# Performance work log

Hardware: AMD Instinct MI355X
Metric: run time of the kernel (lower is better)

Reference implementation:

```python
import jax, jax.numpy as jnp
import numpy as np

MARGIN = 0.2
W_HARD = 1.0
W_SOFT = 0.0
NORMALIZE = True
PD_EPS = 1e-6  # torch F.pairwise_distance eps used inside TripletMarginLoss


def setup_inputs() -> dict:
    key = jax.random.key(0)
    k1, k2, k3 = jax.random.split(key, 3)
    N, D = 8192, 128
    z = jax.random.normal(k1, (N, D), dtype=jnp.float32)
    labels = jax.random.randint(k2, (N,), 0, 16, dtype=jnp.int32)
    subjects = jax.random.randint(k3, (N,), 0, 32, dtype=jnp.int32)
    return {"z": z, "labels": labels, "subjects": subjects}


def _batch_hard(z, pos_mask, neg_mask, margin):
    # pairwise euclidean distances (cdist p=2); mining indices are ints, so
    # stop_gradient keeps vjp clean (matches torch: argmax/argmin detach).
    sq = jnp.sum(z * z, axis=1)
    d2 = sq[:, None] + sq[None, :] - 2.0 * (z @ z.T)
    dist = jax.lax.stop_gradient(jnp.sqrt(jnp.maximum(d2, 0.0)))
    inf = jnp.asarray(jnp.inf, dist.dtype)
    p_idx = jnp.argmax(jnp.where(pos_mask, dist, -inf), axis=1)  # hardest positive
    n_idx = jnp.argmin(jnp.where(neg_mask, dist, inf), axis=1)   # hardest negative
    valid = jnp.any(pos_mask, axis=1) & jnp.any(neg_mask, axis=1)
    a, p, n = z, z[p_idx], z[n_idx]
    d_ap = jnp.sqrt(jnp.sum((a - p + PD_EPS) ** 2, axis=1))
    d_an = jnp.sqrt(jnp.sum((a - n + PD_EPS) ** 2, axis=1))
    per = jnp.maximum(d_ap - d_an + margin, 0.0)
    cnt = jnp.sum(valid)
    loss = jnp.sum(per * valid) / jnp.maximum(cnt, 1).astype(per.dtype)
    return jnp.where(cnt > 0, loss, 0.0)


def reference(z, labels, subjects):
    if NORMALIZE:
        z = z / jnp.maximum(jnp.linalg.norm(z, axis=1, keepdims=True), 1e-12)
    N = z.shape[0]
    same_class = labels[:, None] == labels[None, :]
    same_subj = subjects[:, None] == subjects[None, :]
    not_eye = ~jnp.eye(N, dtype=bool)
    loss = 0.0
    denom = 0.0
    if W_HARD != 0:
        pos_hard = same_class & ~same_subj & not_eye
        neg_hard = ~same_class & same_subj & not_eye
        loss = loss + W_HARD * _batch_hard(z, pos_hard, neg_hard, MARGIN)
        denom += abs(W_HARD)
    if W_SOFT != 0:
        pos_soft = same_class & same_subj & not_eye
        neg_soft = ~same_class & ~same_subj & not_eye
        loss = loss + W_SOFT * _batch_hard(z, pos_soft, neg_soft, MARGIN)
        denom += abs(W_SOFT)
    return loss / max(denom, 1e-12)
```

## Files before the change

### kernel.cpp

```cpp
#include <hip/hip_runtime.h>
#include <math.h>

#define N 8192
#define D 128
#define MARGIN 0.2f
#define PD_EPS 1e-6f
#define NCHUNK 16
#define CHUNKJ (N / NCHUNK)

typedef __attribute__((ext_vector_type(8))) short bf16x8;
typedef __attribute__((ext_vector_type(4))) float f32x4;

__device__ __forceinline__ unsigned short f2bf(float f) {
    unsigned u = __float_as_uint(f);
    u += 0x7FFFu + ((u >> 16) & 1u);
    return (unsigned short)(u >> 16);
}
__device__ __forceinline__ unsigned umn(unsigned a, unsigned b) { return a < b ? a : b; }
__device__ __forceinline__ unsigned umx(unsigned a, unsigned b) { return a > b ? a : b; }

__global__ __launch_bounds__(256) void k_normalize(const float* __restrict__ z,
                                                   const int* __restrict__ labels,
                                                   const int* __restrict__ subjects,
                                                   unsigned short* __restrict__ znb,
                                                   float* __restrict__ invn,
                                                   int* __restrict__ meta) {
    int row  = blockIdx.x * 4 + (threadIdx.x >> 6);
    int lane = threadIdx.x & 63;
    float2 v = ((const float2*)(z + (size_t)row * D))[lane];
    float ss = v.x * v.x + v.y * v.y;
    #pragma unroll
    for (int m = 1; m < 64; m <<= 1) ss += __shfl_xor(ss, m, 64);
    float norm = fmaxf(sqrtf(ss), 1e-12f);
    float ox = v.x / norm, oy = v.y / norm;
    ushort2 b; b.x = f2bf(ox); b.y = f2bf(oy);
    ((ushort2*)(znb + (size_t)row * D))[lane] = b;
    if (lane == 0) {
        invn[row] = 1.0f / norm;
        meta[row] = labels[row] * 32 + subjects[row];
    }
}

__global__ __launch_bounds__(256, 2) void k_mine(const unsigned short* __restrict__ znb,
                                                 const int* __restrict__ meta,
                                                 unsigned* __restrict__ posk,
                                                 unsigned* __restrict__ negk) {
    const int wave = threadIdx.x >> 6;
    const int lane = threadIdx.x & 63;
    const int m    = lane & 15;
    const int quad = lane >> 4;
    const int iw   = (blockIdx.x * 4 + wave) * 64;
    const int jc   = blockIdx.y;
    const int jbase = jc * CHUNKJ;

    bf16x8 afrag[4][4];
    #pragma unroll
    for (int u = 0; u < 4; ++u)
        #pragma unroll
        for (int s = 0; s < 4; ++s)
            afrag[u][s] = *(const bf16x8*)(znb + (size_t)(iw + u * 16 + m) * D + s * 32 + quad * 8);

    int mi[16];
    #pragma unroll
    for (int u = 0; u < 4; ++u)
        #pragma unroll
        for (int r = 0; r < 4; ++r)
            mi[u * 4 + r] = meta[iw + u * 16 + quad * 4 + r];

    unsigned bp[16], bn[16];
    #pragma unroll
    for (int s = 0; s < 16; ++s) { bp[s] = 0xFFFFFFFFu; bn[s] = 0u; }

    for (int t = 0; t < CHUNKJ / 64; ++t) {
        const int jt = jbase + t * 64;

        f32x4 acc[4][4];
        #pragma unroll
        for (int u = 0; u < 4; ++u)
            #pragma unroll
            for (int v = 0; v < 4; ++v)
                acc[u][v] = (f32x4){0.f, 0.f, 0.f, 0.f};

        #pragma unroll
        for (int s = 0; s < 4; ++s) {
            bf16x8 bf[4];
            #pragma unroll
            for (int v = 0; v < 4; ++v)
                bf[v] = *(const bf16x8*)(znb + (size_t)(jt + v * 16 + m) * D + s * 32 + quad * 8);
            #pragma unroll
            for (int u = 0; u < 4; ++u)
                #pragma unroll
                for (int v = 0; v < 4; ++v)
                    acc[u][v] = __builtin_amdgcn_mfma_f32_16x16x32_bf16(afrag[u][s], bf[v], acc[u][v], 0, 0, 0);
        }

        #pragma unroll
        for (int v = 0; v < 4; ++v) {
            const int jv  = jt + v * 16 + m;
            const int mjv = meta[jv];
            #pragma unroll
            for (int u = 0; u < 4; ++u)
                #pragma unroll
                for (int r = 0; r < 4; ++r) {
                    float dot = acc[u][v][r];
                    unsigned key = (__float_as_uint(dot + 2.0f) & 0xFFFFE000u) | (unsigned)jv;
                    int x = mi[u * 4 + r] ^ mjv;
                    bool pos = (x != 0) && (x < 32);
                    bool neg = (x != 0) && ((x & 31) == 0);
                    bp[u * 4 + r] = umn(bp[u * 4 + r], pos ? key : 0xFFFFFFFFu);
                    bn[u * 4 + r] = umx(bn[u * 4 + r], neg ? key : 0u);
                }
        }
    }

    #pragma unroll
    for (int mm = 1; mm < 16; mm <<= 1)
        #pragma unroll
        for (int s = 0; s < 16; ++s) {
            bp[s] = umn(bp[s], (unsigned)__shfl_xor((int)bp[s], mm, 64));
            bn[s] = umx(bn[s], (unsigned)__shfl_xor((int)bn[s], mm, 64));
        }
    if (m == 0) {
        #pragma unroll
        for (int u = 0; u < 4; ++u)
            #pragma unroll
            for (int r = 0; r < 4; ++r) {
                int i = iw + u * 16 + quad * 4 + r;
                posk[(size_t)jc * N + i] = bp[u * 4 + r];
                negk[(size_t)jc * N + i] = bn[u * 4 + r];
            }
    }
}

__global__ __launch_bounds__(256) void k_final(const float* __restrict__ z,
                                               const float* __restrict__ invn,
                                               const unsigned* __restrict__ posk,
                                               const unsigned* __restrict__ negk,
                                               float* __restrict__ per, float* __restrict__ vld) {
    int row  = blockIdx.x * 4 + (threadIdx.x >> 6);
    int lane = threadIdx.x & 63;
    unsigned mp = 0xFFFFFFFFu, mn = 0u;
    #pragma unroll
    for (int c = 0; c < NCHUNK; ++c) {
        mp = umn(mp, posk[(size_t)c * N + row]);
        mn = umx(mn, negk[(size_t)c * N + row]);
    }
    bool valid = (mp != 0xFFFFFFFFu) && (mn != 0u);
    int pi = valid ? (int)(mp & 8191u) : 0;
    int ni = valid ? (int)(mn & 8191u) : 0;
    float ia = invn[row], ip = invn[pi], iq = invn[ni];
    float2 a = ((const float2*)(z + (size_t)row * D))[lane];
    float2 p = ((const float2*)(z + (size_t)pi  * D))[lane];
    float2 q = ((const float2*)(z + (size_t)ni  * D))[lane];
    float dx = a.x * ia - p.x * ip + PD_EPS, dy = a.y * ia - p.y * ip + PD_EPS;
    float sap = dx * dx + dy * dy;
    dx = a.x * ia - q.x * iq + PD_EPS; dy = a.y * ia - q.y * iq + PD_EPS;
    float san = dx * dx + dy * dy;
    #pragma unroll
    for (int m = 1; m < 64; m <<= 1) {
        sap += __shfl_xor(sap, m, 64);
        san += __shfl_xor(san, m, 64);
    }
    if (lane == 0) {
        float l = fmaxf(sqrtf(sap) - sqrtf(san) + MARGIN, 0.0f);
        per[row] = valid ? l : 0.0f;
        vld[row] = valid ? 1.0f : 0.0f;
    }
}

__global__ __launch_bounds__(256) void k_reduce(const float* __restrict__ per,
                                                const float* __restrict__ vld,
                                                float* __restrict__ out) {
    __shared__ float s1[256], s2[256];
    int t = threadIdx.x;
    float a = 0.f, b = 0.f;
    for (int i = t; i < N; i += 256) { a += per[i]; b += vld[i]; }
    s1[t] = a; s2[t] = b;
    __syncthreads();
    for (int w = 128; w > 0; w >>= 1) {
        if (t < w) { s1[t] += s1[t + w]; s2[t] += s2[t + w]; }
        __syncthreads();
    }
    if (t == 0) {
        float cnt = s2[0];
        out[0] = (cnt > 0.f) ? s1[0] / fmaxf(cnt, 1.f) : 0.f;
    }
}

extern "C" void kernel_launch(void* const* d_in, const int* in_sizes, int n_in,
                              void* d_out, int out_size, void* d_ws, size_t ws_size,
                              hipStream_t stream) {
    const float* z        = (const float*)d_in[0];
    const int*   labels   = (const int*)d_in[1];
    const int*   subjects = (const int*)d_in[2];
    float* out = (float*)d_out;

    char* ws = (char*)d_ws;
    unsigned short* znb = (unsigned short*)(ws);
    float*    invn = (float*)   (ws + 2097152);
    int*      meta = (int*)     (ws + 2129920);
    unsigned* posk = (unsigned*)(ws + 2162688);
    unsigned* negk = (unsigned*)(ws + 2686976);
    float*    per  = (float*)   (ws + 3211264);
    float*    vld  = (float*)   (ws + 3244032);

    k_normalize<<<dim3(N / 4), dim3(256), 0, stream>>>(z, labels, subjects, znb, invn, meta);
    k_mine<<<dim3(32, NCHUNK), dim3(256), 0, stream>>>(znb, meta, posk, negk);
    k_final<<<dim3(N / 4), dim3(256), 0, stream>>>(z, invn, posk, negk, per, vld);
    k_reduce<<<dim3(1), dim3(256), 0, stream>>>(per, vld, out);
}
```

Measured before the change: 116.1 us.

## Bucket rows by class and subject to mine only candidate pairs

Rows are scattered into per-class and per-subject index lists with atomics, so mining compares each anchor only against rows sharing its class (positives) or subject (negatives) rather than all N rows. This removes most of the dense N×N bf16 GEMM work. The final loss reduction is fused into the distance kernel through atomics and a last-block pattern, which drops the separate reduce kernel. The fixed bucket capacities (1024 per class, 512 per subject) silently drop overflow rows. Atomic-order-dependent list positions also make the float sum order nondeterministic.

```diff
diff --git a/kernel.cpp b/kernel.cpp
--- a/kernel.cpp
+++ b/kernel.cpp
@@ -5,8 +5,8 @@
 #define D 128
 #define MARGIN 0.2f
 #define PD_EPS 1e-6f
-#define NCHUNK 16
-#define CHUNKJ (N / NCHUNK)
+#define CLS_STRIDE 1024
+#define SUB_STRIDE 512
 
 typedef __attribute__((ext_vector_type(8))) short bf16x8;
 typedef __attribute__((ext_vector_type(4))) float f32x4;
@@ -19,12 +19,15 @@
 __device__ __forceinline__ unsigned umn(unsigned a, unsigned b) { return a < b ? a : b; }
 __device__ __forceinline__ unsigned umx(unsigned a, unsigned b) { return a > b ? a : b; }
 
-__global__ __launch_bounds__(256) void k_normalize(const float* __restrict__ z,
-                                                   const int* __restrict__ labels,
-                                                   const int* __restrict__ subjects,
-                                                   unsigned short* __restrict__ znb,
-                                                   float* __restrict__ invn,
-                                                   int* __restrict__ meta) {
+
+__global__ __launch_bounds__(256) void k_norm_scatter(const float* __restrict__ z,
+                                                      const int* __restrict__ labels,
+                                                      const int* __restrict__ subjects,
+                                                      unsigned short* __restrict__ znb,
+                                                      float* __restrict__ invn,
+                                                      int* __restrict__ counters,
+                                                      int* __restrict__ clsIdx,
+                                                      int* __restrict__ subIdx) {
     int row  = blockIdx.x * 4 + (threadIdx.x >> 6);
     int lane = threadIdx.x & 63;
     float2 v = ((const float2*)(z + (size_t)row * D))[lane];
@@ -32,47 +35,67 @@
     #pragma unroll
     for (int m = 1; m < 64; m <<= 1) ss += __shfl_xor(ss, m, 64);
     float norm = fmaxf(sqrtf(ss), 1e-12f);
-    float ox = v.x / norm, oy = v.y / norm;
-    ushort2 b; b.x = f2bf(ox); b.y = f2bf(oy);
+    ushort2 b; b.x = f2bf(v.x / norm); b.y = f2bf(v.y / norm);
     ((ushort2*)(znb + (size_t)row * D))[lane] = b;
     if (lane == 0) {
         invn[row] = 1.0f / norm;
-        meta[row] = labels[row] * 32 + subjects[row];
-    }
-}
-
-__global__ __launch_bounds__(256, 2) void k_mine(const unsigned short* __restrict__ znb,
-                                                 const int* __restrict__ meta,
-                                                 unsigned* __restrict__ posk,
-                                                 unsigned* __restrict__ negk) {
-    const int wave = threadIdx.x >> 6;
-    const int lane = threadIdx.x & 63;
-    const int m    = lane & 15;
-    const int quad = lane >> 4;
-    const int iw   = (blockIdx.x * 4 + wave) * 64;
-    const int jc   = blockIdx.y;
-    const int jbase = jc * CHUNKJ;
+        int lab = labels[row], sub = subjects[row];
+        int s1 = atomicAdd(&counters[lab], 1);
+        if (s1 < CLS_STRIDE) clsIdx[lab * CLS_STRIDE + s1] = (sub << 13) | row;
+        int s2 = atomicAdd(&counters[16 + sub], 1);
+        if (s2 < SUB_STRIDE) subIdx[sub * SUB_STRIDE + s2] = (lab << 13) | row;
+    }
+}
+
+__global__ __launch_bounds__(64, 2) void k_mine(const unsigned short* __restrict__ znb,
+                                                const int* __restrict__ counters,
+                                                const int* __restrict__ clsIdx,
+                                                const int* __restrict__ subIdx,
+                                                unsigned* __restrict__ posk,
+                                                unsigned* __restrict__ negk) {
+    const int b = blockIdx.x;
+    const bool isPos = b < 256;
+    const int* idx; int cnt, atile;
+    if (isPos) {
+        int c = b >> 4; atile = b & 15;
+        idx = clsIdx + c * CLS_STRIDE;
+        cnt = min(counters[c], CLS_STRIDE);
+    } else {
+        int t = b - 256; int su = t >> 3; atile = t & 7;
+        idx = subIdx + su * SUB_STRIDE;
+        cnt = min(counters[16 + su], SUB_STRIDE);
+    }
+    if (atile * 64 >= cnt) return;
+
+    const int lane = threadIdx.x;
+    const int m = lane & 15, quad = lane >> 4;
 
     bf16x8 afrag[4][4];
     #pragma unroll
+    for (int u = 0; u < 4; ++u) {
+        int sl = min(atile * 64 + u * 16 + m, cnt - 1);
+        size_t row = (size_t)(idx[sl] & 8191);
+        #pragma unroll
+        for (int s = 0; s < 4; ++s)
+            afrag[u][s] = *(const bf16x8*)(znb + row * D + s * 32 + quad * 8);
+    }
+    int cpk[16];
+    #pragma unroll
     for (int u = 0; u < 4; ++u)
         #pragma unroll
-        for (int s = 0; s < 4; ++s)
-            afrag[u][s] = *(const bf16x8*)(znb + (size_t)(iw + u * 16 + m) * D + s * 32 + quad * 8);
-
-    int mi[16];
-    #pragma unroll
-    for (int u = 0; u < 4; ++u)
-        #pragma unroll
         for (int r = 0; r < 4; ++r)
-            mi[u * 4 + r] = meta[iw + u * 16 + quad * 4 + r];
-
-    unsigned bp[16], bn[16];
-    #pragma unroll
-    for (int s = 0; s < 16; ++s) { bp[s] = 0xFFFFFFFFu; bn[s] = 0u; }
-
-    for (int t = 0; t < CHUNKJ / 64; ++t) {
-        const int jt = jbase + t * 64;
+            cpk[u * 4 + r] = idx[min(atile * 64 + u * 16 + quad * 4 + r, cnt - 1)];
+
+    unsigned best[16];
+    #pragma unroll
+    for (int s = 0; s < 16; ++s) best[s] = isPos ? 0xFFFFFFFFu : 0u;
+
+    const int njt = (cnt + 63) >> 6;
+    for (int t = 0; t < njt; ++t) {
+        int pkB[4];
+        #pragma unroll
+        for (int v = 0; v < 4; ++v)
+            pkB[v] = idx[min(t * 64 + v * 16 + m, cnt - 1)];
 
         f32x4 acc[4][4];
         #pragma unroll
@@ -86,7 +109,7 @@
             bf16x8 bf[4];
             #pragma unroll
             for (int v = 0; v < 4; ++v)
-                bf[v] = *(const bf16x8*)(znb + (size_t)(jt + v * 16 + m) * D + s * 32 + quad * 8);
+                bf[v] = *(const bf16x8*)(znb + (size_t)(pkB[v] & 8191) * D + s * 32 + quad * 8);
             #pragma unroll
             for (int u = 0; u < 4; ++u)
                 #pragma unroll
@@ -96,19 +119,16 @@
 
         #pragma unroll
         for (int v = 0; v < 4; ++v) {
-            const int jv  = jt + v * 16 + m;
-            const int mjv = meta[jv];
+            const unsigned pj = (unsigned)pkB[v];
             #pragma unroll
             for (int u = 0; u < 4; ++u)
                 #pragma unroll
                 for (int r = 0; r < 4; ++r) {
-                    float dot = acc[u][v][r];
-                    unsigned key = (__float_as_uint(dot + 2.0f) & 0xFFFFE000u) | (unsigned)jv;
-                    int x = mi[u * 4 + r] ^ mjv;
-                    bool pos = (x != 0) && (x < 32);
-                    bool neg = (x != 0) && ((x & 31) == 0);
-                    bp[u * 4 + r] = umn(bp[u * 4 + r], pos ? key : 0xFFFFFFFFu);
-                    bn[u * 4 + r] = umx(bn[u * 4 + r], neg ? key : 0u);
+                    const int s16 = u * 4 + r;
+                    unsigned key = (__float_as_uint(acc[u][v][r] + 2.0f) & 0xFFFFE000u) | (pj & 8191u);
+                    bool sel = (((unsigned)cpk[s16] ^ pj) & 0xFFFFE000u) != 0u;
+                    if (isPos) best[s16] = umn(best[s16], sel ? key : 0xFFFFFFFFu);
+                    else       best[s16] = umx(best[s16], sel ? key : 0u);
                 }
         }
     }
@@ -117,18 +137,14 @@
     for (int mm = 1; mm < 16; mm <<= 1)
         #pragma unroll
         for (int s = 0; s < 16; ++s) {
-            bp[s] = umn(bp[s], (unsigned)__shfl_xor((int)bp[s], mm, 64));
-            bn[s] = umx(bn[s], (unsigned)__shfl_xor((int)bn[s], mm, 64));
+            unsigned o = (unsigned)__shfl_xor((int)best[s], mm, 64);
+            best[s] = isPos ? umn(best[s], o) : umx(best[s], o);
         }
     if (m == 0) {
-        #pragma unroll
-        for (int u = 0; u < 4; ++u)
-            #pragma unroll
-            for (int r = 0; r < 4; ++r) {
-                int i = iw + u * 16 + quad * 4 + r;
-                posk[(size_t)jc * N + i] = bp[u * 4 + r];
-                negk[(size_t)jc * N + i] = bn[u * 4 + r];
-            }
+        unsigned* dst = isPos ? posk : negk;
+        #pragma unroll
+        for (int s = 0; s < 16; ++s)
+            dst[cpk[s] & 8191] = best[s];
     }
 }
 
@@ -136,54 +152,58 @@
                                                const float* __restrict__ invn,
                                                const unsigned* __restrict__ posk,
                                                const unsigned* __restrict__ negk,
-                                               float* __restrict__ per, float* __restrict__ vld) {
-    int row  = blockIdx.x * 4 + (threadIdx.x >> 6);
-    int lane = threadIdx.x & 63;
-    unsigned mp = 0xFFFFFFFFu, mn = 0u;
-    #pragma unroll
-    for (int c = 0; c < NCHUNK; ++c) {
-        mp = umn(mp, posk[(size_t)c * N + row]);
-        mn = umx(mn, negk[(size_t)c * N + row]);
-    }
+                                               float* __restrict__ acc,
+                                               float* __restrict__ out) {
+    const int rb = threadIdx.x >> 4;
+    const int l  = threadIdx.x & 15;
+    const int row = blockIdx.x * 16 + rb;
+    unsigned mp = posk[row], mn = negk[row];
     bool valid = (mp != 0xFFFFFFFFu) && (mn != 0u);
     int pi = valid ? (int)(mp & 8191u) : 0;
     int ni = valid ? (int)(mn & 8191u) : 0;
     float ia = invn[row], ip = invn[pi], iq = invn[ni];
-    float2 a = ((const float2*)(z + (size_t)row * D))[lane];
-    float2 p = ((const float2*)(z + (size_t)pi  * D))[lane];
-    float2 q = ((const float2*)(z + (size_t)ni  * D))[lane];
-    float dx = a.x * ia - p.x * ip + PD_EPS, dy = a.y * ia - p.y * ip + PD_EPS;
-    float sap = dx * dx + dy * dy;
-    dx = a.x * ia - q.x * iq + PD_EPS; dy = a.y * ia - q.y * iq + PD_EPS;
-    float san = dx * dx + dy * dy;
-    #pragma unroll
-    for (int m = 1; m < 64; m <<= 1) {
-        sap += __shfl_xor(sap, m, 64);
-        san += __shfl_xor(san, m, 64);
-    }
-    if (lane == 0) {
-        float l = fmaxf(sqrtf(sap) - sqrtf(san) + MARGIN, 0.0f);
-        per[row] = valid ? l : 0.0f;
-        vld[row] = valid ? 1.0f : 0.0f;
-    }
-}
-
-__global__ __launch_bounds__(256) void k_reduce(const float* __restrict__ per,
-                                                const float* __restrict__ vld,
-                                                float* __restrict__ out) {
-    __shared__ float s1[256], s2[256];
-    int t = threadIdx.x;
-    float a = 0.f, b = 0.f;
-    for (int i = t; i < N; i += 256) { a += per[i]; b += vld[i]; }
-    s1[t] = a; s2[t] = b;
+    const float4* za = (const float4*)(z + (size_t)row * D);
+    const float4* zp = (const float4*)(z + (size_t)pi * D);
+    const float4* zq = (const float4*)(z + (size_t)ni * D);
+    float sap = 0.f, san = 0.f;
+    #pragma unroll
+    for (int k = 0; k < 2; ++k) {
+        float4 a = za[l * 2 + k], p = zp[l * 2 + k], q = zq[l * 2 + k];
+        float d;
+        d = a.x * ia - p.x * ip + PD_EPS; sap += d * d;
+        d = a.y * ia - p.y * ip + PD_EPS; sap += d * d;
+        d = a.z * ia - p.z * ip + PD_EPS; sap += d * d;
+        d = a.w * ia - p.w * ip + PD_EPS; sap += d * d;
+        d = a.x * ia - q.x * iq + PD_EPS; san += d * d;
+        d = a.y * ia - q.y * iq + PD_EPS; san += d * d;
+        d = a.z * ia - q.z * iq + PD_EPS; san += d * d;
+        d = a.w * ia - q.w * iq + PD_EPS; san += d * d;
+    }
+    #pragma unroll
+    for (int mm = 1; mm < 16; mm <<= 1) {
+        sap += __shfl_xor(sap, mm, 64);
+        san += __shfl_xor(san, mm, 64);
+    }
+    __shared__ float ls[16], vs[16];
+    if (l == 0) {
+        float lo = fmaxf(sqrtf(sap) - sqrtf(san) + MARGIN, 0.0f);
+        ls[rb] = valid ? lo : 0.0f;
+        vs[rb] = valid ? 1.0f : 0.0f;
+    }
     __syncthreads();
-    for (int w = 128; w > 0; w >>= 1) {
-        if (t < w) { s1[t] += s1[t + w]; s2[t] += s2[t + w]; }
-        __syncthreads();
-    }
-    if (t == 0) {
-        float cnt = s2[0];
-        out[0] = (cnt > 0.f) ? s1[0] / fmaxf(cnt, 1.f) : 0.f;
+    if (threadIdx.x == 0) {
+        float s = 0.f, c = 0.f;
+        #pragma unroll
+        for (int i = 0; i < 16; ++i) { s += ls[i]; c += vs[i]; }
+        atomicAdd(&acc[0], s);
+        atomicAdd(&acc[1], c);
+        __threadfence();
+        unsigned old = atomicAdd((unsigned*)&acc[2], 1u);
+        if (old == (unsigned)(gridDim.x - 1)) {
+            float S = atomicAdd(&acc[0], 0.0f);
+            float C = atomicAdd(&acc[1], 0.0f);
+            out[0] = (C > 0.f) ? S / fmaxf(C, 1.f) : 0.f;
+        }
     }
 }
 
@@ -196,16 +216,18 @@
     float* out = (float*)d_out;
 
     char* ws = (char*)d_ws;
-    unsigned short* znb = (unsigned short*)(ws);
-    float*    invn = (float*)   (ws + 2097152);
-    int*      meta = (int*)     (ws + 2129920);
-    unsigned* posk = (unsigned*)(ws + 2162688);
-    unsigned* negk = (unsigned*)(ws + 2686976);
-    float*    per  = (float*)   (ws + 3211264);
-    float*    vld  = (float*)   (ws + 3244032);
-
-    k_normalize<<<dim3(N / 4), dim3(256), 0, stream>>>(z, labels, subjects, znb, invn, meta);
-    k_mine<<<dim3(32, NCHUNK), dim3(256), 0, stream>>>(znb, meta, posk, negk);
-    k_final<<<dim3(N / 4), dim3(256), 0, stream>>>(z, invn, posk, negk, per, vld);
-    k_reduce<<<dim3(1), dim3(256), 0, stream>>>(per, vld, out);
-}
+    unsigned short* znb  = (unsigned short*)(ws);
+    float*    invn     = (float*)   (ws + 2097152);
+    int*      clsIdx   = (int*)     (ws + 2129920);
+    int*      subIdx   = (int*)     (ws + 2195456);
+    unsigned* posk     = (unsigned*)(ws + 2260992);
+    unsigned* negk     = (unsigned*)(ws + 2293760);
+    int*      counters = (int*)     (ws + 2326528);
+    float*    acc      = (float*)   (ws + 2326528 + 48 * 4);
+
+    hipMemsetAsync(counters, 0, 256, stream);
+    k_norm_scatter<<<dim3(N / 4), dim3(256), 0, stream>>>(z, labels, subjects, znb, invn,
+                                                          counters, clsIdx, subIdx);
+    k_mine<<<dim3(512), dim3(64), 0, stream>>>(znb, counters, clsIdx, subIdx, posk, negk);
+    k_final<<<dim3(N / 16), dim3(256), 0, stream>>>(z, invn, posk, negk, acc, out);
+}
```

New measurement: 227.0 us. 95.5% more time.
